# Kernel tuning notes

Hardware: AMD Instinct MI355X
Metric: run time of the kernel (lower is better)

## Reference

```python
import jax, jax.numpy as jnp
import numpy as np

INPUTDIM = 256
OUTDIM = 256
GRIDSIZE = 300
SCALE_BASE = 1.0
SCALE_FOURIER = 1.0
BATCH = 2048


def setup_inputs() -> dict:
    key = jax.random.key(0)
    k_x, k_bw, k_fc = jax.random.split(key, 3)
    x = jax.random.normal(k_x, (BATCH, INPUTDIM), dtype=jnp.float32)
    # HeUniform for base_weight: limit = sqrt(6 / fan_in)
    limit = np.sqrt(6.0 / INPUTDIM)
    base_weight = jax.random.uniform(
        k_bw, (INPUTDIM, OUTDIM), dtype=jnp.float32, minval=-limit, maxval=limit)
    stddev = 1.0 / (np.sqrt(INPUTDIM) * np.sqrt(GRIDSIZE))
    fouriercoeffs = (jax.random.normal(k_fc, (2, OUTDIM, INPUTDIM, GRIDSIZE), dtype=jnp.float32)
                     * jnp.float32(stddev))
    return {"x": x, "base_weight": base_weight, "fouriercoeffs": fouriercoeffs}


def reference(x, base_weight, fouriercoeffs):
    # Base path: silu(x @ W)
    base_output = jax.nn.silu(x @ base_weight)  # [B, J]
    # Fourier feature expansion: k = 1..gridsize
    k = jnp.arange(1, GRIDSIZE + 1, dtype=x.dtype)  # [K]
    theta = x[:, :, None] * k[None, None, :]        # [B, I, K]
    c = jnp.cos(theta)
    s = jnp.sin(theta)
    # einsum 'dbik,djik->bj' split into cos and sin parts
    fourier_output = (jnp.einsum('bik,jik->bj', c, fouriercoeffs[0])
                      + jnp.einsum('bik,jik->bj', s, fouriercoeffs[1]))
    return SCALE_BASE * base_output + SCALE_FOURIER * fourier_output
```

## Files before the change

### kernel.cpp

```cpp
#include <hip/hip_runtime.h>
#include <hip/hip_bf16.h>
#include <cstdint>

#define BATCH   2048
#define INDIM   256
#define OUTDIM  256
#define KGRID   300
#define NCHUNK  10

typedef __attribute__((ext_vector_type(4))) float f32x4;
typedef __attribute__((ext_vector_type(2))) float f32x2;
typedef __attribute__((ext_vector_type(8))) short bf16x8;

__device__ __forceinline__ uint32_t pack_bf16x2(float lo, float hi) {
    union { __hip_bfloat162 h; uint32_t u; } cv;
    cv.h = __float22bfloat162_rn(make_float2(lo, hi));
    return cv.u;
}

__device__ __forceinline__ f32x2 pk_fma_sub(f32x2 a, f32x2 b, f32x2 c) {
    f32x2 d;
    asm("v_pk_fma_f32 %0, %1, %2, %3 neg_lo:[0,0,1] neg_hi:[0,0,1]"
        : "=v"(d) : "v"(a), "v"(b), "v"(c));
    return d;
}

__device__ __forceinline__ void load_lds16(const void* g, void* l) {
    __builtin_amdgcn_global_load_lds(
        (const __attribute__((address_space(1))) void*)g,
        (__attribute__((address_space(3))) void*)l, 16, 0, 0);
}

__device__ __forceinline__ bf16x8 zero_frag() {
    union { uint32_t u[4]; bf16x8 v; } z = {{0u, 0u, 0u, 0u}};
    return z.v;
}

__device__ __forceinline__ bf16x8 gen_frag(float ck, float sk,
                                           float c1, float s1) {
    float cp = __builtin_fmaf(ck, c1,  sk * s1);
    float sp = __builtin_fmaf(sk, c1, -ck * s1);
    f32x2 C; C.x = ck; C.y = sk;
    f32x2 P; P.x = cp; P.y = sp;
    f32x2 T2; T2.x = c1 + c1; T2.y = c1 + c1;
    union { uint32_t u[4]; bf16x8 v; } r;
    #pragma unroll
    for (int q = 0; q < 4; ++q) {
        r.u[q] = pack_bf16x2(C.x, C.y);
        f32x2 N = pk_fma_sub(T2, C, P);
        P = C; C = N;
    }
    return r.v;
}

#define PACKED_U4 ((size_t)INDIM * NCHUNK * OUTDIM * 8)
#define PACKED_BYTES (PACKED_U4 * 16)

__global__ __launch_bounds__(256) void pack_kernel(
    const float* __restrict__ fc, uint4* __restrict__ pk)
{
    size_t tidg = (size_t)blockIdx.x * 256 + threadIdx.x;
    int sub = tidg & 7;
    int j   = (tidg >> 3) & 255;
    int ich = (int)(tidg >> 11);
    int ch  = ich % NCHUNK;
    int i   = ich / NCHUNK;
    int kb  = ch * 32 + (sub ^ (j & 7)) * 4;
    if (kb > KGRID - 4) kb = KGRID - 4;
    const float* pc = fc + ((size_t)j * INDIM + i) * KGRID + kb;
    const float* ps = pc + (size_t)OUTDIM * INDIM * KGRID;
    float4 vc = *reinterpret_cast<const float4*>(pc);
    float4 vs = *reinterpret_cast<const float4*>(ps);
    uint4 wv;
    wv.x = pack_bf16x2(vc.x, vs.x);
    wv.y = pack_bf16x2(vc.y, vs.y);
    wv.z = pack_bf16x2(vc.z, vs.z);
    wv.w = pack_bf16x2(vc.w, vs.w);
    pk[tidg] = wv;
}

__global__ __launch_bounds__(256, 2) void fourier_dma_kernel(
    const float* __restrict__ x, const uint4* __restrict__ pk,
    float* __restrict__ part)
{
    __shared__ uint4 Bbuf[2][256][8];

    const int tid = threadIdx.x;
    const int flat = blockIdx.x + (blockIdx.z << 4);
    const int L  = (flat & 7) * 64 + (flat >> 3);
    const int b0 = (L & 15) * 128;
    const int z  = L >> 4;
    const int i0 = z * 8;

    const int lane = tid & 63, wave = tid >> 6;
    const int wm = wave >> 1, wn = wave & 1;
    const int lrow = lane & 15, lgrp = lane >> 4;
    const int q8 = wave * 8;

    f32x4 acc[2][4][4] = {};

    float thn[4];
    float c1[4], s1[4];
    float c16[4], s16[4];
    float cS[4], sS[4];

    #pragma unroll
    for (int mf = 0; mf < 4; ++mf)
        thn[mf] = x[(size_t)(b0 + wm * 64 + mf * 16 + lrow) * INDIM + i0];

    {
        const uint4* src = pk + (size_t)(i0 * NCHUNK) * 2048;
        char* dst = (char*)&Bbuf[0][0][0];
        #pragma unroll
        for (int q = 0; q < 8; ++q)
            load_lds16(src + (q8 + q) * 64 + lane, dst + (q8 + q) * 1024);
    }

    int il = 0, ch = 0;
    #pragma unroll 1
    for (int t = 0; t < 8 * NCHUNK; ++t) {
        {
            int il2 = il, ch2 = ch + 1;
            if (ch2 == NCHUNK) { ch2 = 0; il2 = (il + 1 < 8) ? il + 1 : il; }
            const uint4* src = pk + (size_t)((i0 + il2) * NCHUNK + ch2) * 2048;
            char* dst = (char*)&Bbuf[(t + 1) & 1][0][0];
            #pragma unroll
            for (int q = 0; q < 8; ++q)
                load_lds16(src + (q8 + q) * 64 + lane, dst + (q8 + q) * 1024);
        }
        if (ch == 0) {
            const float flg = (float)(lgrp * 4);
            #pragma unroll
            for (int mf = 0; mf < 4; ++mf) {
                float th = thn[mf];
                __sincosf(th, &s1[mf], &c1[mf]);
                __sincosf(16.f * th, &s16[mf], &c16[mf]);
                float a0 = __builtin_fmaf(flg, th, th);
                __sincosf(a0, &sS[mf], &cS[mf]);
            }
            int iln = (il + 1 < 8) ? il + 1 : il;
            #pragma unroll
            for (int mf = 0; mf < 4; ++mf)
                thn[mf] = x[(size_t)(b0 + wm * 64 + mf * 16 + lrow) * INDIM
                            + i0 + iln];
        }
        bf16x8 af[2][4];
        #pragma unroll
        for (int mf = 0; mf < 4; ++mf) {
            af[0][mf] = gen_frag(cS[mf], sS[mf], c1[mf], s1[mf]);
            float ck = __builtin_fmaf(cS[mf], c16[mf], -sS[mf] * s16[mf]);
            float sk = __builtin_fmaf(sS[mf], c16[mf],  cS[mf] * s16[mf]);
            af[1][mf] = gen_frag(ck, sk, c1[mf], s1[mf]);
            cS[mf] = __builtin_fmaf(ck, c16[mf], -sk * s16[mf]);
            sS[mf] = __builtin_fmaf(sk, c16[mf],  ck * s16[mf]);
        }
        if (ch == NCHUNK - 1) {
            #pragma unroll
            for (int mf = 0; mf < 4; ++mf) {
                af[0][mf] = (lgrp == 3) ? zero_frag() : af[0][mf];
                af[1][mf] = zero_frag();
            }
        }
        __syncthreads();
        __builtin_amdgcn_s_setprio(1);
        #pragma unroll
        for (int s = 0; s < 2; ++s) {
            #pragma unroll
            for (int ns = 0; ns < 2; ++ns) {
                bf16x8 bfr[4];
                #pragma unroll
                for (int nf = 0; nf < 4; ++nf) {
                    const int jl = wn * 128 + ns * 64 + nf * 16 + lrow;
                    uint4 tv = Bbuf[t & 1][jl][(s * 4 + lgrp) ^ (jl & 7)];
                    bfr[nf] = *reinterpret_cast<bf16x8*>(&tv);
                }
                #pragma unroll
                for (int mf = 0; mf < 4; ++mf)
                    #pragma unroll
                    for (int nf = 0; nf < 4; ++nf)
                        acc[ns][mf][nf] = __builtin_amdgcn_mfma_f32_16x16x32_bf16(
                            af[s][mf], bfr[nf], acc[ns][mf][nf], 0, 0, 0);
            }
        }
        __builtin_amdgcn_s_setprio(0);
        __syncthreads();
        if (++ch == NCHUNK) { ch = 0; ++il; }
    }

    float* pws = part + (size_t)z * BATCH * OUTDIM;
    #pragma unroll
    for (int ns = 0; ns < 2; ++ns)
        #pragma unroll
        for (int mf = 0; mf < 4; ++mf)
            #pragma unroll
            for (int nf = 0; nf < 4; ++nf)
                #pragma unroll
                for (int r = 0; r < 4; ++r) {
                    int b = b0 + wm * 64 + mf * 16 + lgrp * 4 + r;
                    int j = wn * 128 + ns * 64 + nf * 16 + lrow;
                    pws[(size_t)b * OUTDIM + j] = acc[ns][mf][nf][r];
                }
}

__global__ __launch_bounds__(256, 2) void fourier_kernel_fb(
    const float* __restrict__ x, const float* __restrict__ fc,
    float* __restrict__ ws, int ips)
{
    __shared__ uint4 Abuf[2][128][8];
    __shared__ uint4 Bbuf[128][8];

    const int tid  = threadIdx.x;
    const int b0   = blockIdx.x * 256;
    const int j0   = blockIdx.y * 128;
    const int i0   = blockIdx.z * ips;

    const int lane = tid & 63, wave = tid >> 6;
    const int wm   = wave >> 1, wn = wave & 1;
    const int lrow = lane & 15, lgrp = lane >> 4;
    const int grow = tid >> 1,  gh = tid & 1;

    f32x4 acc[2][4][4] = {};

    #pragma unroll 1
    for (int il = 0; il < ips; ++il) {
        const int i = i0 + il;
        float th[2], c1[2], s1[2], t2[2];
        th[0] = x[(size_t)(b0 + grow)       * INDIM + i];
        th[1] = x[(size_t)(b0 + 128 + grow) * INDIM + i];
        #pragma unroll
        for (int m = 0; m < 2; ++m) {
            __sincosf(th[m], &s1[m], &c1[m]);
            t2[m] = 2.f * c1[m];
        }
        #pragma unroll 1
        for (int ch = 0; ch < NCHUNK; ++ch) {
            #pragma unroll
            for (int r = 0; r < 4; ++r) {
                int flat = r * 256 + tid;
                int jl = flat >> 3, sub = flat & 7;
                int kb = ch * 32 + sub * 4;
                if (kb > KGRID - 4) kb = KGRID - 4;
                const float* pc = fc + ((size_t)(j0 + jl) * INDIM + i) * KGRID + kb;
                const float* ps = pc + (size_t)OUTDIM * INDIM * KGRID;
                float4 vc = *reinterpret_cast<const float4*>(pc);
                float4 vs = *reinterpret_cast<const float4*>(ps);
                uint4 wv;
                wv.x = pack_bf16x2(vc.x, vs.x);
                wv.y = pack_bf16x2(vc.y, vs.y);
                wv.z = pack_bf16x2(vc.z, vs.z);
                wv.w = pack_bf16x2(vc.w, vs.w);
                Bbuf[jl][sub ^ (jl & 7)] = wv;
            }
            #pragma unroll
            for (int m = 0; m < 2; ++m) {
                const int k0 = ch * 32 + gh * 16;
                float ck, sk;
                __sincosf(th[m] * (float)(k0 + 1), &sk, &ck);
                float cp = __builtin_fmaf(ck, c1[m],  sk * s1[m]);
                float sp = __builtin_fmaf(sk, c1[m], -ck * s1[m]);
                const int swz = grow & 7;
                #pragma unroll
                for (int c = 0; c < 4; ++c) {
                    uint32_t uu[4];
                    #pragma unroll
                    for (int qq = 0; qq < 4; ++qq) {
                        const int kidx = k0 + c * 4 + qq;
                        float cc = (kidx < KGRID) ? ck : 0.f;
                        float ss = (kidx < KGRID) ? sk : 0.f;
                        uu[qq] = pack_bf16x2(cc, ss);
                        float cn = __builtin_fmaf(t2[m], ck, -cp);
                        float sn = __builtin_fmaf(t2[m], sk, -sp);
                        cp = ck; sp = sk; ck = cn; sk = sn;
                    }
                    Abuf[m][grow][(gh * 4 + c) ^ swz] =
                        make_uint4(uu[0], uu[1], uu[2], uu[3]);
                }
            }
            __syncthreads();
            #pragma unroll
            for (int s = 0; s < 2; ++s) {
                bf16x8 bfr[4];
                #pragma unroll
                for (int nf = 0; nf < 4; ++nf) {
                    const int jl = wn * 64 + nf * 16 + lrow;
                    uint4 tv = Bbuf[jl][(s * 4 + lgrp) ^ (jl & 7)];
                    bfr[nf] = *reinterpret_cast<bf16x8*>(&tv);
                }
                #pragma unroll
                for (int m = 0; m < 2; ++m) {
                    #pragma unroll
                    for (int mf = 0; mf < 4; ++mf) {
                        const int rowA = wm * 64 + mf * 16 + lrow;
                        uint4 tv = Abuf[m][rowA][(s * 4 + lgrp) ^ (rowA & 7)];
                        bf16x8 af = *reinterpret_cast<bf16x8*>(&tv);
                        #pragma unroll
                        for (int nf = 0; nf < 4; ++nf)
                            acc[m][mf][nf] = __builtin_amdgcn_mfma_f32_16x16x32_bf16(
                                af, bfr[nf], acc[m][mf][nf], 0, 0, 0);
                    }
                }
            }
            __syncthreads();
        }
    }

    float* pws = ws + (size_t)blockIdx.z * BATCH * OUTDIM;
    #pragma unroll
    for (int m = 0; m < 2; ++m)
        #pragma unroll
        for (int mf = 0; mf < 4; ++mf)
            #pragma unroll
            for (int nf = 0; nf < 4; ++nf)
                #pragma unroll
                for (int r = 0; r < 4; ++r) {
                    int b = b0 + m * 128 + wm * 64 + mf * 16 + lgrp * 4 + r;
                    int j = j0 + wn * 64 + nf * 16 + lrow;
                    pws[(size_t)b * OUTDIM + j] = acc[m][mf][nf][r];
                }
}

__global__ __launch_bounds__(256) void combine_kernel(
    const float* __restrict__ x, const float* __restrict__ w,
    const float* __restrict__ part, float* __restrict__ out, int nsplit)
{
    __shared__ float Xs[64][16];
    __shared__ float Wt[16][68];

    const int tid = threadIdx.x;
    const int b0 = blockIdx.x * 64;
    const int j0 = blockIdx.y * 64;
    const int tx = tid & 15, ty = tid >> 4;

    float acc[4][4] = {};

    for (int kb = 0; kb < INDIM; kb += 16) {
        {
            int m = tid >> 2, kq = (tid & 3) * 4;
            float4 v = *reinterpret_cast<const float4*>(
                &x[(size_t)(b0 + m) * INDIM + kb + kq]);
            Xs[m][kq+0] = v.x; Xs[m][kq+1] = v.y; Xs[m][kq+2] = v.z; Xs[m][kq+3] = v.w;
        }
        {
            int kr = tid >> 4, jc = (tid & 15) * 4;
            float4 v = *reinterpret_cast<const float4*>(
                &w[(size_t)(kb + kr) * OUTDIM + j0 + jc]);
            Wt[kr][jc+0] = v.x; Wt[kr][jc+1] = v.y; Wt[kr][jc+2] = v.z; Wt[kr][jc+3] = v.w;
        }
        __syncthreads();
        #pragma unroll
        for (int kk = 0; kk < 16; ++kk) {
            float a[4], b[4];
            #pragma unroll
            for (int q = 0; q < 4; ++q) { a[q] = Xs[ty*4+q][kk]; b[q] = Wt[kk][tx*4+q]; }
            #pragma unroll
            for (int q = 0; q < 4; ++q)
                #pragma unroll
                for (int p = 0; p < 4; ++p)
                    acc[q][p] = __builtin_fmaf(a[q], b[p], acc[q][p]);
        }
        __syncthreads();
    }

    float psum[4][4] = {};
    for (int s = 0; s < nsplit; ++s) {
        const float* base = part + (size_t)s * BATCH * OUTDIM;
        #pragma unroll
        for (int q = 0; q < 4; ++q) {
            float4 pv = *reinterpret_cast<const float4*>(
                &base[(size_t)(b0 + ty*4 + q) * OUTDIM + j0 + tx*4]);
            psum[q][0] += pv.x; psum[q][1] += pv.y;
            psum[q][2] += pv.z; psum[q][3] += pv.w;
        }
    }

    #pragma unroll
    for (int q = 0; q < 4; ++q)
        #pragma unroll
        for (int p = 0; p < 4; ++p) {
            float v = acc[q][p];
            float sv = v / (1.f + __expf(-v));
            out[(size_t)(b0 + ty*4 + q) * OUTDIM + (j0 + tx*4 + p)] =
                sv + psum[q][p];
        }
}

extern "C" void kernel_launch(void* const* d_in, const int* in_sizes, int n_in,
                              void* d_out, int out_size, void* d_ws, size_t ws_size,
                              hipStream_t stream) {
    const float* x  = (const float*)d_in[0];
    const float* bw = (const float*)d_in[1];
    const float* fc = (const float*)d_in[2];
    float* out = (float*)d_out;

    const size_t per = (size_t)BATCH * OUTDIM * sizeof(float);

    if (ws_size >= PACKED_BYTES + 32 * per) {
        uint4* pk   = (uint4*)d_ws;
        float* part = (float*)((char*)d_ws + PACKED_BYTES);
        pack_kernel<<<(int)(PACKED_U4 / 256), 256, 0, stream>>>(fc, pk);
        fourier_dma_kernel<<<dim3(16, 1, 32), 256, 0, stream>>>(x, pk, part);
        combine_kernel<<<dim3(BATCH / 64, OUTDIM / 64), 256, 0, stream>>>(
            x, bw, part, out, 32);
    } else {
        float* part = (float*)d_ws;
        int S = 32;
        while (S > 1 && (size_t)S * per > ws_size) S >>= 1;
        const int ips = INDIM / S;
        fourier_kernel_fb<<<dim3(BATCH / 256, OUTDIM / 128, S), 256, 0, stream>>>(
            x, fc, part, ips);
        combine_kernel<<<dim3(BATCH / 64, OUTDIM / 64), 256, 0, stream>>>(
            x, bw, part, out, S);
    }
}
```

Baseline: 252.8 us.

## Load packed Fourier weights directly into registers instead of via LDS double buffer

```diff
diff --git a/kernel.cpp b/kernel.cpp
--- a/kernel.cpp
+++ b/kernel.cpp
@@ -23,12 +23,6 @@
     asm("v_pk_fma_f32 %0, %1, %2, %3 neg_lo:[0,0,1] neg_hi:[0,0,1]"
         : "=v"(d) : "v"(a), "v"(b), "v"(c));
     return d;
-}
-
-__device__ __forceinline__ void load_lds16(const void* g, void* l) {
-    __builtin_amdgcn_global_load_lds(
-        (const __attribute__((address_space(1))) void*)g,
-        (__attribute__((address_space(3))) void*)l, 16, 0, 0);
 }
 
 __device__ __forceinline__ bf16x8 zero_frag() {
@@ -60,12 +54,15 @@
     const float* __restrict__ fc, uint4* __restrict__ pk)
 {
     size_t tidg = (size_t)blockIdx.x * 256 + threadIdx.x;
-    int sub = tidg & 7;
-    int j   = (tidg >> 3) & 255;
-    int ich = (int)(tidg >> 11);
-    int ch  = ich % NCHUNK;
-    int i   = ich / NCHUNK;
-    int kb  = ch * 32 + (sub ^ (j & 7)) * 4;
+    int lrow = tidg & 15;
+    int lgrp = (int)(tidg >> 4) & 3;
+    int jb   = (int)(tidg >> 6) & 15;
+    int s    = (int)(tidg >> 10) & 1;
+    int ich  = (int)(tidg >> 11);
+    int ch   = ich % NCHUNK;
+    int i    = ich / NCHUNK;
+    int j    = jb * 16 + lrow;
+    int kb   = ch * 32 + (s * 4 + lgrp) * 4;
     if (kb > KGRID - 4) kb = KGRID - 4;
     const float* pc = fc + ((size_t)j * INDIM + i) * KGRID + kb;
     const float* ps = pc + (size_t)OUTDIM * INDIM * KGRID;
@@ -79,12 +76,10 @@
     pk[tidg] = wv;
 }
 
-__global__ __launch_bounds__(256, 2) void fourier_dma_kernel(
+__global__ __launch_bounds__(256, 2) void fourier_reg_kernel(
     const float* __restrict__ x, const uint4* __restrict__ pk,
     float* __restrict__ part)
 {
-    __shared__ uint4 Bbuf[2][256][8];
-
     const int tid = threadIdx.x;
     const int flat = blockIdx.x + (blockIdx.z << 4);
     const int L  = (flat & 7) * 64 + (flat >> 3);
@@ -95,7 +90,6 @@
     const int lane = tid & 63, wave = tid >> 6;
     const int wm = wave >> 1, wn = wave & 1;
     const int lrow = lane & 15, lgrp = lane >> 4;
-    const int q8 = wave * 8;
 
     f32x4 acc[2][4][4] = {};
 
@@ -108,26 +102,12 @@
     for (int mf = 0; mf < 4; ++mf)
         thn[mf] = x[(size_t)(b0 + wm * 64 + mf * 16 + lrow) * INDIM + i0];
 
-    {
-        const uint4* src = pk + (size_t)(i0 * NCHUNK) * 2048;
-        char* dst = (char*)&Bbuf[0][0][0];
-        #pragma unroll
-        for (int q = 0; q < 8; ++q)
-            load_lds16(src + (q8 + q) * 64 + lane, dst + (q8 + q) * 1024);
-    }
+    const uint4* bbase = pk + (size_t)(i0 * NCHUNK) * 2048
+                            + wn * 512 + lgrp * 16 + lrow;
 
     int il = 0, ch = 0;
     #pragma unroll 1
     for (int t = 0; t < 8 * NCHUNK; ++t) {
-        {
-            int il2 = il, ch2 = ch + 1;
-            if (ch2 == NCHUNK) { ch2 = 0; il2 = (il + 1 < 8) ? il + 1 : il; }
-            const uint4* src = pk + (size_t)((i0 + il2) * NCHUNK + ch2) * 2048;
-            char* dst = (char*)&Bbuf[(t + 1) & 1][0][0];
-            #pragma unroll
-            for (int q = 0; q < 8; ++q)
-                load_lds16(src + (q8 + q) * 64 + lane, dst + (q8 + q) * 1024);
-        }
         if (ch == 0) {
             const float flg = (float)(lgrp * 4);
             #pragma unroll
@@ -161,7 +141,6 @@
                 af[1][mf] = zero_frag();
             }
         }
-        __syncthreads();
         __builtin_amdgcn_s_setprio(1);
         #pragma unroll
         for (int s = 0; s < 2; ++s) {
@@ -170,8 +149,7 @@
                 bf16x8 bfr[4];
                 #pragma unroll
                 for (int nf = 0; nf < 4; ++nf) {
-                    const int jl = wn * 128 + ns * 64 + nf * 16 + lrow;
-                    uint4 tv = Bbuf[t & 1][jl][(s * 4 + lgrp) ^ (jl & 7)];
+                    uint4 tv = bbase[s * 1024 + (ns * 4 + nf) * 64];
                     bfr[nf] = *reinterpret_cast<bf16x8*>(&tv);
                 }
                 #pragma unroll
@@ -183,7 +161,7 @@
             }
         }
         __builtin_amdgcn_s_setprio(0);
-        __syncthreads();
+        bbase += 2048;
         if (++ch == NCHUNK) { ch = 0; ++il; }
     }
 
@@ -398,7 +376,7 @@
         uint4* pk   = (uint4*)d_ws;
         float* part = (float*)((char*)d_ws + PACKED_BYTES);
         pack_kernel<<<(int)(PACKED_U4 / 256), 256, 0, stream>>>(fc, pk);
-        fourier_dma_kernel<<<dim3(16, 1, 32), 256, 0, stream>>>(x, pk, part);
+        fourier_reg_kernel<<<dim3(16, 1, 32), 256, 0, stream>>>(x, pk, part);
         combine_kernel<<<dim3(BATCH / 64, OUTDIM / 64), 256, 0, stream>>>(
             x, bw, part, out, 32);
     } else {
```

Result: slower. 274.5 us (+8.6%).

## Remap waves to 32 rows by full 256 columns in Fourier MFMA kernel

Applied to the files above, without the earlier changes.

```diff
diff --git a/kernel.cpp b/kernel.cpp
--- a/kernel.cpp
+++ b/kernel.cpp
@@ -93,20 +93,20 @@
     const int i0 = z * 8;
 
     const int lane = tid & 63, wave = tid >> 6;
-    const int wm = wave >> 1, wn = wave & 1;
+    const int wrow = wave * 32;
     const int lrow = lane & 15, lgrp = lane >> 4;
     const int q8 = wave * 8;
 
-    f32x4 acc[2][4][4] = {};
-
-    float thn[4];
-    float c1[4], s1[4];
-    float c16[4], s16[4];
-    float cS[4], sS[4];
+    f32x4 acc[2][16] = {};
+
+    float thn[2];
+    float c1[2], s1[2];
+    float c16[2], s16[2];
+    float cS[2], sS[2];
 
     #pragma unroll
-    for (int mf = 0; mf < 4; ++mf)
-        thn[mf] = x[(size_t)(b0 + wm * 64 + mf * 16 + lrow) * INDIM + i0];
+    for (int mf = 0; mf < 2; ++mf)
+        thn[mf] = x[(size_t)(b0 + wrow + mf * 16 + lrow) * INDIM + i0];
 
     {
         const uint4* src = pk + (size_t)(i0 * NCHUNK) * 2048;
@@ -131,7 +131,7 @@
         if (ch == 0) {
             const float flg = (float)(lgrp * 4);
             #pragma unroll
-            for (int mf = 0; mf < 4; ++mf) {
+            for (int mf = 0; mf < 2; ++mf) {
                 float th = thn[mf];
                 __sincosf(th, &s1[mf], &c1[mf]);
                 __sincosf(16.f * th, &s16[mf], &c16[mf]);
@@ -140,13 +140,13 @@
             }
             int iln = (il + 1 < 8) ? il + 1 : il;
             #pragma unroll
-            for (int mf = 0; mf < 4; ++mf)
-                thn[mf] = x[(size_t)(b0 + wm * 64 + mf * 16 + lrow) * INDIM
+            for (int mf = 0; mf < 2; ++mf)
+                thn[mf] = x[(size_t)(b0 + wrow + mf * 16 + lrow) * INDIM
                             + i0 + iln];
         }
-        bf16x8 af[2][4];
-        #pragma unroll
-        for (int mf = 0; mf < 4; ++mf) {
+        bf16x8 af[2][2];
+        #pragma unroll
+        for (int mf = 0; mf < 2; ++mf) {
             af[0][mf] = gen_frag(cS[mf], sS[mf], c1[mf], s1[mf]);
             float ck = __builtin_fmaf(cS[mf], c16[mf], -sS[mf] * s16[mf]);
             float sk = __builtin_fmaf(sS[mf], c16[mf],  cS[mf] * s16[mf]);
@@ -156,7 +156,7 @@
         }
         if (ch == NCHUNK - 1) {
             #pragma unroll
-            for (int mf = 0; mf < 4; ++mf) {
+            for (int mf = 0; mf < 2; ++mf) {
                 af[0][mf] = (lgrp == 3) ? zero_frag() : af[0][mf];
                 af[1][mf] = zero_frag();
             }
@@ -165,21 +165,22 @@
         __builtin_amdgcn_s_setprio(1);
         #pragma unroll
         for (int s = 0; s < 2; ++s) {
-            #pragma unroll
-            for (int ns = 0; ns < 2; ++ns) {
+            const int swz = (s * 4 + lgrp) ^ (lrow & 7);
+            #pragma unroll
+            for (int g = 0; g < 4; ++g) {
                 bf16x8 bfr[4];
                 #pragma unroll
-                for (int nf = 0; nf < 4; ++nf) {
-                    const int jl = wn * 128 + ns * 64 + nf * 16 + lrow;
-                    uint4 tv = Bbuf[t & 1][jl][(s * 4 + lgrp) ^ (jl & 7)];
-                    bfr[nf] = *reinterpret_cast<bf16x8*>(&tv);
+                for (int q = 0; q < 4; ++q) {
+                    const int jl = (g * 4 + q) * 16 + lrow;
+                    uint4 tv = Bbuf[t & 1][jl][swz];
+                    bfr[q] = *reinterpret_cast<bf16x8*>(&tv);
                 }
                 #pragma unroll
-                for (int mf = 0; mf < 4; ++mf)
+                for (int mf = 0; mf < 2; ++mf)
                     #pragma unroll
-                    for (int nf = 0; nf < 4; ++nf)
-                        acc[ns][mf][nf] = __builtin_amdgcn_mfma_f32_16x16x32_bf16(
-                            af[s][mf], bfr[nf], acc[ns][mf][nf], 0, 0, 0);
+                    for (int q = 0; q < 4; ++q)
+                        acc[mf][g * 4 + q] = __builtin_amdgcn_mfma_f32_16x16x32_bf16(
+                            af[s][mf], bfr[q], acc[mf][g * 4 + q], 0, 0, 0);
             }
         }
         __builtin_amdgcn_s_setprio(0);
@@ -189,17 +190,15 @@
 
     float* pws = part + (size_t)z * BATCH * OUTDIM;
     #pragma unroll
-    for (int ns = 0; ns < 2; ++ns)
-        #pragma unroll
-        for (int mf = 0; mf < 4; ++mf)
-            #pragma unroll
-            for (int nf = 0; nf < 4; ++nf)
-                #pragma unroll
-                for (int r = 0; r < 4; ++r) {
-                    int b = b0 + wm * 64 + mf * 16 + lgrp * 4 + r;
-                    int j = wn * 128 + ns * 64 + nf * 16 + lrow;
-                    pws[(size_t)b * OUTDIM + j] = acc[ns][mf][nf][r];
-                }
+    for (int mf = 0; mf < 2; ++mf)
+        #pragma unroll
+        for (int nf = 0; nf < 16; ++nf)
+            #pragma unroll
+            for (int r = 0; r < 4; ++r) {
+                int b = b0 + wrow + mf * 16 + lgrp * 4 + r;
+                int j = nf * 16 + lrow;
+                pws[(size_t)b * OUTDIM + j] = acc[mf][nf][r];
+            }
 }
 
 __global__ __launch_bounds__(256, 2) void fourier_kernel_fb(
```

Measured after the change: 223.6 us. 11.6% less time.

## Retile Fourier MFMA kernel to 256x128 blocks with half-size LDS B tile

Applied to the files above, without the earlier changes.

```diff
diff --git a/kernel.cpp b/kernel.cpp
--- a/kernel.cpp
+++ b/kernel.cpp
@@ -83,21 +83,22 @@
     const float* __restrict__ x, const uint4* __restrict__ pk,
     float* __restrict__ part)
 {
-    __shared__ uint4 Bbuf[2][256][8];
+    __shared__ uint4 Bbuf[2][128][8];
 
     const int tid = threadIdx.x;
-    const int flat = blockIdx.x + (blockIdx.z << 4);
+    const int flat = blockIdx.x + (blockIdx.y << 3) + (blockIdx.z << 4);
     const int L  = (flat & 7) * 64 + (flat >> 3);
-    const int b0 = (L & 15) * 128;
+    const int b0 = (L & 7) * 256;
+    const int j0 = ((L >> 3) & 1) * 128;
     const int z  = L >> 4;
     const int i0 = z * 8;
 
     const int lane = tid & 63, wave = tid >> 6;
-    const int wm = wave >> 1, wn = wave & 1;
+    const int wrow = wave * 64;
     const int lrow = lane & 15, lgrp = lane >> 4;
-    const int q8 = wave * 8;
-
-    f32x4 acc[2][4][4] = {};
+    const int q4 = wave * 4;
+
+    f32x4 acc[4][8] = {};
 
     float thn[4];
     float c1[4], s1[4];
@@ -106,14 +107,14 @@
 
     #pragma unroll
     for (int mf = 0; mf < 4; ++mf)
-        thn[mf] = x[(size_t)(b0 + wm * 64 + mf * 16 + lrow) * INDIM + i0];
+        thn[mf] = x[(size_t)(b0 + wrow + mf * 16 + lrow) * INDIM + i0];
 
     {
-        const uint4* src = pk + (size_t)(i0 * NCHUNK) * 2048;
+        const uint4* src = pk + (size_t)(i0 * NCHUNK) * 2048 + j0 * 8;
         char* dst = (char*)&Bbuf[0][0][0];
         #pragma unroll
-        for (int q = 0; q < 8; ++q)
-            load_lds16(src + (q8 + q) * 64 + lane, dst + (q8 + q) * 1024);
+        for (int q = 0; q < 4; ++q)
+            load_lds16(src + (q4 + q) * 64 + lane, dst + (q4 + q) * 1024);
     }
 
     int il = 0, ch = 0;
@@ -122,11 +123,12 @@
         {
             int il2 = il, ch2 = ch + 1;
             if (ch2 == NCHUNK) { ch2 = 0; il2 = (il + 1 < 8) ? il + 1 : il; }
-            const uint4* src = pk + (size_t)((i0 + il2) * NCHUNK + ch2) * 2048;
+            const uint4* src =
+                pk + (size_t)((i0 + il2) * NCHUNK + ch2) * 2048 + j0 * 8;
             char* dst = (char*)&Bbuf[(t + 1) & 1][0][0];
             #pragma unroll
-            for (int q = 0; q < 8; ++q)
-                load_lds16(src + (q8 + q) * 64 + lane, dst + (q8 + q) * 1024);
+            for (int q = 0; q < 4; ++q)
+                load_lds16(src + (q4 + q) * 64 + lane, dst + (q4 + q) * 1024);
         }
         if (ch == 0) {
             const float flg = (float)(lgrp * 4);
@@ -141,45 +143,70 @@
             int iln = (il + 1 < 8) ? il + 1 : il;
             #pragma unroll
             for (int mf = 0; mf < 4; ++mf)
-                thn[mf] = x[(size_t)(b0 + wm * 64 + mf * 16 + lrow) * INDIM
+                thn[mf] = x[(size_t)(b0 + wrow + mf * 16 + lrow) * INDIM
                             + i0 + iln];
         }
-        bf16x8 af[2][4];
+        bf16x8 af[4];
         #pragma unroll
         for (int mf = 0; mf < 4; ++mf) {
-            af[0][mf] = gen_frag(cS[mf], sS[mf], c1[mf], s1[mf]);
-            float ck = __builtin_fmaf(cS[mf], c16[mf], -sS[mf] * s16[mf]);
-            float sk = __builtin_fmaf(sS[mf], c16[mf],  cS[mf] * s16[mf]);
-            af[1][mf] = gen_frag(ck, sk, c1[mf], s1[mf]);
-            cS[mf] = __builtin_fmaf(ck, c16[mf], -sk * s16[mf]);
-            sS[mf] = __builtin_fmaf(sk, c16[mf],  ck * s16[mf]);
-        }
-        if (ch == NCHUNK - 1) {
-            #pragma unroll
-            for (int mf = 0; mf < 4; ++mf) {
-                af[0][mf] = (lgrp == 3) ? zero_frag() : af[0][mf];
-                af[1][mf] = zero_frag();
-            }
+            af[mf] = gen_frag(cS[mf], sS[mf], c1[mf], s1[mf]);
+            float cn = __builtin_fmaf(cS[mf], c16[mf], -sS[mf] * s16[mf]);
+            float sn = __builtin_fmaf(sS[mf], c16[mf],  cS[mf] * s16[mf]);
+            cS[mf] = cn; sS[mf] = sn;
+        }
+        if (ch == NCHUNK - 1 && lgrp == 3) {
+            #pragma unroll
+            for (int mf = 0; mf < 4; ++mf) af[mf] = zero_frag();
         }
         __syncthreads();
         __builtin_amdgcn_s_setprio(1);
-        #pragma unroll
-        for (int s = 0; s < 2; ++s) {
-            #pragma unroll
-            for (int ns = 0; ns < 2; ++ns) {
+        {
+            const int swz = lgrp ^ (lrow & 7);
+            #pragma unroll
+            for (int g = 0; g < 2; ++g) {
                 bf16x8 bfr[4];
                 #pragma unroll
-                for (int nf = 0; nf < 4; ++nf) {
-                    const int jl = wn * 128 + ns * 64 + nf * 16 + lrow;
-                    uint4 tv = Bbuf[t & 1][jl][(s * 4 + lgrp) ^ (jl & 7)];
-                    bfr[nf] = *reinterpret_cast<bf16x8*>(&tv);
+                for (int q = 0; q < 4; ++q) {
+                    const int jl = (g * 4 + q) * 16 + lrow;
+                    uint4 tv = Bbuf[t & 1][jl][swz];
+                    bfr[q] = *reinterpret_cast<bf16x8*>(&tv);
                 }
                 #pragma unroll
                 for (int mf = 0; mf < 4; ++mf)
                     #pragma unroll
-                    for (int nf = 0; nf < 4; ++nf)
-                        acc[ns][mf][nf] = __builtin_amdgcn_mfma_f32_16x16x32_bf16(
-                            af[s][mf], bfr[nf], acc[ns][mf][nf], 0, 0, 0);
+                    for (int q = 0; q < 4; ++q)
+                        acc[mf][g * 4 + q] = __builtin_amdgcn_mfma_f32_16x16x32_bf16(
+                            af[mf], bfr[q], acc[mf][g * 4 + q], 0, 0, 0);
+            }
+        }
+        #pragma unroll
+        for (int mf = 0; mf < 4; ++mf) {
+            af[mf] = gen_frag(cS[mf], sS[mf], c1[mf], s1[mf]);
+            float cn = __builtin_fmaf(cS[mf], c16[mf], -sS[mf] * s16[mf]);
+            float sn = __builtin_fmaf(sS[mf], c16[mf],  cS[mf] * s16[mf]);
+            cS[mf] = cn; sS[mf] = sn;
+        }
+        if (ch == NCHUNK - 1) {
+            #pragma unroll
+            for (int mf = 0; mf < 4; ++mf) af[mf] = zero_frag();
+        }
+        {
+            const int swz = (4 + lgrp) ^ (lrow & 7);
+            #pragma unroll
+            for (int g = 0; g < 2; ++g) {
+                bf16x8 bfr[4];
+                #pragma unroll
+                for (int q = 0; q < 4; ++q) {
+                    const int jl = (g * 4 + q) * 16 + lrow;
+                    uint4 tv = Bbuf[t & 1][jl][swz];
+                    bfr[q] = *reinterpret_cast<bf16x8*>(&tv);
+                }
+                #pragma unroll
+                for (int mf = 0; mf < 4; ++mf)
+                    #pragma unroll
+                    for (int q = 0; q < 4; ++q)
+                        acc[mf][g * 4 + q] = __builtin_amdgcn_mfma_f32_16x16x32_bf16(
+                            af[mf], bfr[q], acc[mf][g * 4 + q], 0, 0, 0);
             }
         }
         __builtin_amdgcn_s_setprio(0);
@@ -189,17 +216,15 @@
 
     float* pws = part + (size_t)z * BATCH * OUTDIM;
     #pragma unroll
-    for (int ns = 0; ns < 2; ++ns)
-        #pragma unroll
-        for (int mf = 0; mf < 4; ++mf)
-            #pragma unroll
-            for (int nf = 0; nf < 4; ++nf)
-                #pragma unroll
-                for (int r = 0; r < 4; ++r) {
-                    int b = b0 + wm * 64 + mf * 16 + lgrp * 4 + r;
-                    int j = wn * 128 + ns * 64 + nf * 16 + lrow;
-                    pws[(size_t)b * OUTDIM + j] = acc[ns][mf][nf][r];
-                }
+    for (int mf = 0; mf < 4; ++mf)
+        #pragma unroll
+        for (int nf = 0; nf < 8; ++nf)
+            #pragma unroll
+            for (int r = 0; r < 4; ++r) {
+                int b = b0 + wrow + mf * 16 + lgrp * 4 + r;
+                int j = j0 + nf * 16 + lrow;
+                pws[(size_t)b * OUTDIM + j] = acc[mf][nf][r];
+            }
 }
 
 __global__ __launch_bounds__(256, 2) void fourier_kernel_fb(
@@ -398,7 +423,7 @@
         uint4* pk   = (uint4*)d_ws;
         float* part = (float*)((char*)d_ws + PACKED_BYTES);
         pack_kernel<<<(int)(PACKED_U4 / 256), 256, 0, stream>>>(fc, pk);
-        fourier_dma_kernel<<<dim3(16, 1, 32), 256, 0, stream>>>(x, pk, part);
+        fourier_dma_kernel<<<dim3(8, 2, 32), 256, 0, stream>>>(x, pk, part);
         combine_kernel<<<dim3(BATCH / 64, OUTDIM / 64), 256, 0, stream>>>(
             x, bw, part, out, 32);
     } else {
```

New measurement: 254.4 us. About the same (+0.6%).
